# Performance work log

Hardware: AMD Instinct MI355X
Metric: run time of the kernel (lower is better)

Reference implementation:

```python
import jax, jax.numpy as jnp
import numpy as np

EPS = 1e-06

def setup_inputs() -> dict:
    key = jax.random.key(0)
    k1, k2, k3 = jax.random.split(key, 3)
    N, L, H, D = 4, 4096, 16, 64
    return {
        "queries": jax.random.normal(k1, (N, L, H, D), dtype=jnp.float32),
        "keys": jax.random.normal(k2, (N, L, H, D), dtype=jnp.float32),
        "values": jax.random.normal(k3, (N, L, H, D), dtype=jnp.float32),
    }

def reference(queries, keys, values):
    # [N, L, H, D] -> [N, H, L, D]
    q = jnp.transpose(queries, (0, 2, 1, 3))
    k = jnp.transpose(keys, (0, 2, 1, 3))
    v = jnp.transpose(values, (0, 2, 1, 3))
    # kernel feature map
    q = jax.nn.sigmoid(q)
    k = jax.nn.sigmoid(k)
    L = q.shape[2]
    S = k.shape[2]
    # incoming/outgoing flow normalizers
    normalizer_row = 1.0 / jnp.einsum('nhld,nhd->nhl', q + EPS, k.sum(axis=2) + EPS)
    normalizer_col = 1.0 / jnp.einsum('nhsd,nhd->nhs', k + EPS, q.sum(axis=2) + EPS)
    # refined normalizers (competition / allocation)
    row_refine = jnp.einsum('nhld,nhd->nhl', q + EPS,
                            (k * normalizer_col[..., None]).sum(axis=2) + EPS)
    col_refine = jnp.einsum('nhsd,nhd->nhs', k + EPS,
                            (q * normalizer_row[..., None]).sum(axis=2) + EPS)
    row_refine = jax.nn.sigmoid(row_refine * (float(L) / float(S)))
    col_refine = jax.nn.softmax(col_refine, axis=-1) * S
    # linear attention aggregation: kv is [N, H, D, D]
    kv = jnp.einsum('nhsd,nhse->nhde', k, v * col_refine[..., None])
    x = jnp.einsum('nhld,nhde->nhle', q, kv) * (normalizer_row * row_refine)[..., None]
    # back to [N, L, H, D]
    return jnp.transpose(x, (0, 2, 1, 3))
```

## Files before the change

### kernel.cpp

```cpp
#include <hip/hip_runtime.h>
#include <math.h>

#define EPS 1e-6f
constexpr int N_ = 4, L_ = 4096, H_ = 16, D_ = 64;
constexpr int NH = N_ * H_;
constexpr int HD = H_ * D_;
constexpr long NSTRIDE = (long)L_ * HD;
constexpr int SCHUNKS = 16;
constexpr int K1B = 1024;

typedef __attribute__((ext_vector_type(8))) short short8;
typedef __attribute__((ext_vector_type(4))) float f32x4;

__device__ float g_qsum[NH * D_];
__device__ float g_ksum[NH * D_];
__device__ float g_qnr[NH * D_];
__device__ float g_knc[NH * D_];
__device__ float g_ssum[NH];
__device__ float g_kv[NH * D_ * D_];
__device__ float g_kvpart[(long)SCHUNKS * NH * D_ * D_];
__device__ float g_part[2 * K1B * 1024];

__device__ __forceinline__ float sigm(float x) {
    return 1.0f / (1.0f + __expf(-x));
}
__device__ __forceinline__ float4 sigm4(float4 x) {
    float4 r;
    r.x = sigm(x.x); r.y = sigm(x.y); r.z = sigm(x.z); r.w = sigm(x.w);
    return r;
}
__device__ __forceinline__ float red16(float p) {
    p += __shfl_xor(p, 1);
    p += __shfl_xor(p, 2);
    p += __shfl_xor(p, 4);
    p += __shfl_xor(p, 8);
    return p;
}
__device__ __forceinline__ unsigned rne_hi(unsigned xb) {
    return (xb + 0x7fffu + ((xb >> 16) & 1u)) & 0xffff0000u;
}
__device__ __forceinline__ uint2 split2(float x) {
    unsigned h1 = rne_hi(__float_as_uint(x));
    float r = x - __uint_as_float(h1);
    unsigned h2 = rne_hi(__float_as_uint(r));
    return make_uint2(h1, h2);
}
union U8 { unsigned u[4]; short8 s; };

__global__ __launch_bounds__(256) void k1_sums(const float* __restrict__ q,
                                               const float* __restrict__ k) {
    const float* src = blockIdx.z ? k : q;
    int t = threadIdx.x;
    long g0 = (long)blockIdx.x * 16;
    const float* p = src + g0 * HD + t * 4;
    float ax = 0.f, ay = 0.f, az = 0.f, aw = 0.f;
#pragma unroll
    for (int r = 0; r < 16; ++r) {
        float4 x = *(const float4*)(p + (long)r * HD);
        float4 s = sigm4(x);
        ax += s.x; ay += s.y; az += s.z; aw += s.w;
    }
    float4 o = {ax, ay, az, aw};
    *(float4*)&g_part[((blockIdx.z * K1B + blockIdx.x) << 10) + t * 4] = o;
}

__global__ __launch_bounds__(256) void k2_norm(const float* __restrict__ q,
                                               const float* __restrict__ k) {
    bool col = blockIdx.z != 0;
    const float* src = col ? k : q;
    const float* sums = col ? g_qsum : g_ksum;
    int t = threadIdx.x;
    long g0 = (long)blockIdx.x * 16;
    int n = (int)(g0 >> 12);
    float4 bv = *(const float4*)(sums + n * 1024 + t * 4);
    bv.x += EPS; bv.y += EPS; bv.z += EPS; bv.w += EPS;
    const float* p = src + g0 * HD + t * 4;
    float ax = 0.f, ay = 0.f, az = 0.f, aw = 0.f;
#pragma unroll 4
    for (int r = 0; r < 16; ++r) {
        float4 x = *(const float4*)(p + (long)r * HD);
        float4 s = sigm4(x);
        float pd = (s.x + EPS) * bv.x + (s.y + EPS) * bv.y
                 + (s.z + EPS) * bv.z + (s.w + EPS) * bv.w;
        pd = red16(pd);
        float inv = 1.0f / pd;
        ax += s.x * inv; ay += s.y * inv; az += s.z * inv; aw += s.w * inv;
    }
    float4 o = {ax, ay, az, aw};
    *(float4*)&g_part[((blockIdx.z * K1B + blockIdx.x) << 10) + t * 4] = o;
}

__global__ __launch_bounds__(256) void kred(int which) {
    int bid = blockIdx.x, t = threadIdx.x;
    int z = bid & 1, n = (bid >> 1) & 3, cc = bid >> 3;
    int c = cc * 128 + (t & 31) * 4;
    int bg = t >> 5;
    float sx = 0.f, sy = 0.f, sz = 0.f, sw = 0.f;
#pragma unroll 4
    for (int i = 0; i < 32; ++i) {
        int b = n * 256 + bg * 32 + i;
        const float* pp = &g_part[((z * K1B + b) << 10) + c];
        float4 p = *(const float4*)pp;
        sx += p.x; sy += p.y; sz += p.z; sw += p.w;
    }
    __shared__ float4 esb[256];
    esb[t] = make_float4(sx, sy, sz, sw);
    __syncthreads();
    if (t < 32) {
        float4 s = esb[t];
#pragma unroll
        for (int g = 1; g < 8; ++g) {
            float4 b = esb[t + g * 32];
            s.x += b.x; s.y += b.y; s.z += b.z; s.w += b.w;
        }
        float* dst = which ? (z ? g_knc : g_qnr) : (z ? g_ksum : g_qsum);
        *(float4*)&dst[n * 1024 + cc * 128 + t * 4] = s;
    }
    if (which == 0 && bid == 0 && t < NH) g_ssum[t] = 0.f;
}

__global__ __launch_bounds__(256, 4) void k4_kv(const float* __restrict__ k,
                                                const float* __restrict__ v) {
    int nh = blockIdx.y, n = nh >> 4, h = nh & 15;
    int t = threadIdx.x, lane = t & 63, wv = t >> 6;
    __shared__ unsigned kA[16 * 66], kB[16 * 66], vA[16 * 66], vB[16 * 66];
    __shared__ float esb[256];
    int sp = t >> 4, c4 = t & 15;
    long nbase = (long)n * NSTRIDE + (long)h * D_;
    int s0blk = blockIdx.x * 256;
    float4 qn = *(const float4*)&g_qnr[nh * 64 + c4 * 4];
    qn.x += EPS; qn.y += EPS; qn.z += EPS; qn.w += EPS;

    f32x4 acc[4];
#pragma unroll
    for (int e = 0; e < 4; ++e) acc[e] = (f32x4){0.f, 0.f, 0.f, 0.f};
    int m = lane & 15, qd = lane >> 4;
    float esum = 0.f;

    float4 ke, ko, ve, vo;
    {
        long gb = nbase + (long)(s0blk + 2 * sp) * HD + c4 * 4;
        ke = *(const float4*)&k[gb]; ko = *(const float4*)&k[gb + HD];
        ve = *(const float4*)&v[gb]; vo = *(const float4*)&v[gb + HD];
    }
    for (int st = 0; st < 8; ++st) {
        float4 se = sigm4(ke), so = sigm4(ko);
        float pde = (se.x + EPS) * qn.x + (se.y + EPS) * qn.y
                  + (se.z + EPS) * qn.z + (se.w + EPS) * qn.w;
        float pdo = (so.x + EPS) * qn.x + (so.y + EPS) * qn.y
                  + (so.z + EPS) * qn.z + (so.w + EPS) * qn.w;
        pde = red16(pde); pdo = red16(pdo);
        float ee = __expf(pde), eo = __expf(pdo);
        if (c4 == 0) esum += ee + eo;
        se.x *= ee; se.y *= ee; se.z *= ee; se.w *= ee;
        so.x *= eo; so.y *= eo; so.z *= eo; so.w *= eo;
        uint2 a0 = split2(se.x), a1_ = split2(se.y), a2_ = split2(se.z), a3_ = split2(se.w);
        uint2 b0 = split2(so.x), b1_ = split2(so.y), b2_ = split2(so.z), b3_ = split2(so.w);
        unsigned kaw0 = (a0.x >> 16) | (b0.x & 0xffff0000u);
        unsigned kaw1 = (a1_.x >> 16) | (b1_.x & 0xffff0000u);
        unsigned kaw2 = (a2_.x >> 16) | (b2_.x & 0xffff0000u);
        unsigned kaw3 = (a3_.x >> 16) | (b3_.x & 0xffff0000u);
        unsigned kbw0 = (a0.y >> 16) | (b0.y & 0xffff0000u);
        unsigned kbw1 = (a1_.y >> 16) | (b1_.y & 0xffff0000u);
        unsigned kbw2 = (a2_.y >> 16) | (b2_.y & 0xffff0000u);
        unsigned kbw3 = (a3_.y >> 16) | (b3_.y & 0xffff0000u);
        uint2 c0 = split2(ve.x), c1 = split2(ve.y), c2 = split2(ve.z), c3 = split2(ve.w);
        uint2 d0 = split2(vo.x), d1 = split2(vo.y), d2 = split2(vo.z), d3 = split2(vo.w);
        unsigned vaw0 = (c0.x >> 16) | (d0.x & 0xffff0000u);
        unsigned vaw1 = (c1.x >> 16) | (d1.x & 0xffff0000u);
        unsigned vaw2 = (c2.x >> 16) | (d2.x & 0xffff0000u);
        unsigned vaw3 = (c3.x >> 16) | (d3.x & 0xffff0000u);
        unsigned vbw0 = (c0.y >> 16) | (d0.y & 0xffff0000u);
        unsigned vbw1 = (c1.y >> 16) | (d1.y & 0xffff0000u);
        unsigned vbw2 = (c2.y >> 16) | (d2.y & 0xffff0000u);
        unsigned vbw3 = (c3.y >> 16) | (d3.y & 0xffff0000u);
        __syncthreads();
        int wb = sp * 66 + c4 * 4;
        *(uint2*)&kA[wb] = make_uint2(kaw0, kaw1); *(uint2*)&kA[wb + 2] = make_uint2(kaw2, kaw3);
        *(uint2*)&kB[wb] = make_uint2(kbw0, kbw1); *(uint2*)&kB[wb + 2] = make_uint2(kbw2, kbw3);
        *(uint2*)&vA[wb] = make_uint2(vaw0, vaw1); *(uint2*)&vA[wb + 2] = make_uint2(vaw2, vaw3);
        *(uint2*)&vB[wb] = make_uint2(vbw0, vbw1); *(uint2*)&vB[wb + 2] = make_uint2(vbw2, vbw3);
        __syncthreads();
        if (st < 7) {
            long gb = nbase + (long)(s0blk + (st + 1) * 32 + 2 * sp) * HD + c4 * 4;
            ke = *(const float4*)&k[gb]; ko = *(const float4*)&k[gb + HD];
            ve = *(const float4*)&v[gb]; vo = *(const float4*)&v[gb + HD];
        }
        U8 fa1, fa2;
#pragma unroll
        for (int jp = 0; jp < 4; ++jp) {
            int idx = (qd * 4 + jp) * 66 + wv * 16 + m;
            fa1.u[jp] = kA[idx]; fa2.u[jp] = kB[idx];
        }
#pragma unroll
        for (int e = 0; e < 4; ++e) {
            U8 fb1, fb2;
#pragma unroll
            for (int jp = 0; jp < 4; ++jp) {
                int idx = (qd * 4 + jp) * 66 + e * 16 + m;
                fb1.u[jp] = vA[idx]; fb2.u[jp] = vB[idx];
            }
            acc[e] = __builtin_amdgcn_mfma_f32_16x16x32_bf16(fa1.s, fb2.s, acc[e], 0, 0, 0);
            acc[e] = __builtin_amdgcn_mfma_f32_16x16x32_bf16(fa2.s, fb1.s, acc[e], 0, 0, 0);
            acc[e] = __builtin_amdgcn_mfma_f32_16x16x32_bf16(fa1.s, fb1.s, acc[e], 0, 0, 0);
        }
    }
    float* dst = &g_kvpart[((long)blockIdx.x * NH + nh) * 4096];
#pragma unroll
    for (int e = 0; e < 4; ++e)
#pragma unroll
        for (int r = 0; r < 4; ++r)
            dst[(wv * 16 + qd * 4 + r) * 64 + e * 16 + m] = acc[e][r];
    esb[t] = esum;
    __syncthreads();
    for (int s = 128; s; s >>= 1) {
        if (t < s) esb[t] += esb[t + s];
        __syncthreads();
    }
    if (t == 0) atomicAdd(&g_ssum[nh], esb[0]);
}

__global__ __launch_bounds__(256) void k4b_reduce() {
    int nh = blockIdx.x;
    int i4 = blockIdx.y * 256 + threadIdx.x;
    float sx = 0.f, sy = 0.f, sz = 0.f, sw = 0.f;
#pragma unroll
    for (int c = 0; c < SCHUNKS; ++c) {
        float4 p = *(const float4*)&g_kvpart[((long)c * NH + nh) * 4096 + i4 * 4];
        sx += p.x; sy += p.y; sz += p.z; sw += p.w;
    }
    float scale = (float)L_ / g_ssum[nh];
    float4 o = {sx * scale, sy * scale, sz * scale, sw * scale};
    *(float4*)&g_kv[nh * 4096 + i4 * 4] = o;
}

__global__ __launch_bounds__(256, 4) void k5_out(const float* __restrict__ q,
                                                 float* __restrict__ out) {
    int nh = blockIdx.y, n = nh >> 4, h = nh & 15;
    int t = threadIdx.x, lane = t & 63, wv = t >> 6;
    __shared__ unsigned qA[32 * 66], qB[32 * 66], kvA[32 * 66], kvB[32 * 66];
    __shared__ float coef[64];
    int c4 = t & 15;
    long nbase = (long)n * NSTRIDE + (long)h * D_;
    int l0 = blockIdx.x * 64;
    float4 bk1 = *(const float4*)&g_ksum[nh * 64 + c4 * 4];
    float4 bk2 = *(const float4*)&g_knc[nh * 64 + c4 * 4];
    bk1.x += EPS; bk1.y += EPS; bk1.z += EPS; bk1.w += EPS;
    bk2.x += EPS; bk2.y += EPS; bk2.z += EPS; bk2.w += EPS;
#pragma unroll
    for (int j = 0; j < 2; ++j) {
        int slot = t + j * 256;
        int dp = slot >> 4, cc = slot & 15;
        const float* kvr = &g_kv[nh * 4096 + (2 * dp) * 64 + cc * 4];
        float4 xe = *(const float4*)kvr;
        float4 xo = *(const float4*)(kvr + 64);
        uint2 e0 = split2(xe.x), e1 = split2(xe.y), e2 = split2(xe.z), e3 = split2(xe.w);
        uint2 o0 = split2(xo.x), o1 = split2(xo.y), o2 = split2(xo.z), o3 = split2(xo.w);
        int wb = dp * 66 + cc * 4;
        *(uint2*)&kvA[wb] = make_uint2((e0.x >> 16) | (o0.x & 0xffff0000u),
                                       (e1.x >> 16) | (o1.x & 0xffff0000u));
        *(uint2*)&kvA[wb + 2] = make_uint2((e2.x >> 16) | (o2.x & 0xffff0000u),
                                           (e3.x >> 16) | (o3.x & 0xffff0000u));
        *(uint2*)&kvB[wb] = make_uint2((e0.y >> 16) | (o0.y & 0xffff0000u),
                                       (e1.y >> 16) | (o1.y & 0xffff0000u));
        *(uint2*)&kvB[wb + 2] = make_uint2((e2.y >> 16) | (o2.y & 0xffff0000u),
                                           (e3.y >> 16) | (o3.y & 0xffff0000u));
    }
#pragma unroll
    for (int j = 0; j < 4; ++j) {
        int slot = t + j * 256;
        int r = slot >> 4;
        float4 x = *(const float4*)&q[nbase + (long)(l0 + r) * HD + c4 * 4];
        float4 s = sigm4(x);
        float p1 = (s.x + EPS) * bk1.x + (s.y + EPS) * bk1.y
                 + (s.z + EPS) * bk1.z + (s.w + EPS) * bk1.w;
        float p2 = (s.x + EPS) * bk2.x + (s.y + EPS) * bk2.y
                 + (s.z + EPS) * bk2.z + (s.w + EPS) * bk2.w;
        p1 = red16(p1); p2 = red16(p2);
        if (c4 == 0) coef[r] = sigm(p2) / p1;
        uint2 t0 = split2(s.x), t1 = split2(s.y), t2 = split2(s.z), t3 = split2(s.w);
        qA[(c4 * 2) * 66 + r]     = (t0.x >> 16) | (t1.x & 0xffff0000u);
        qB[(c4 * 2) * 66 + r]     = (t0.y >> 16) | (t1.y & 0xffff0000u);
        qA[(c4 * 2 + 1) * 66 + r] = (t2.x >> 16) | (t3.x & 0xffff0000u);
        qB[(c4 * 2 + 1) * 66 + r] = (t2.y >> 16) | (t3.y & 0xffff0000u);
    }
    __syncthreads();
    int m = lane & 15, qd = lane >> 4;
    f32x4 acc[4];
#pragma unroll
    for (int e = 0; e < 4; ++e) acc[e] = (f32x4){0.f, 0.f, 0.f, 0.f};
#pragma unroll
    for (int kk = 0; kk < 2; ++kk) {
        U8 fa1, fa2;
#pragma unroll
        for (int jp = 0; jp < 4; ++jp) {
            int idx = (kk * 16 + qd * 4 + jp) * 66 + wv * 16 + m;
            fa1.u[jp] = qA[idx]; fa2.u[jp] = qB[idx];
        }
#pragma unroll
        for (int e = 0; e < 4; ++e) {
            U8 fb1, fb2;
#pragma unroll
            for (int jp = 0; jp < 4; ++jp) {
                int idx = (kk * 16 + qd * 4 + jp) * 66 + e * 16 + m;
                fb1.u[jp] = kvA[idx]; fb2.u[jp] = kvB[idx];
            }
            acc[e] = __builtin_amdgcn_mfma_f32_16x16x32_bf16(fa1.s, fb2.s, acc[e], 0, 0, 0);
            acc[e] = __builtin_amdgcn_mfma_f32_16x16x32_bf16(fa2.s, fb1.s, acc[e], 0, 0, 0);
            acc[e] = __builtin_amdgcn_mfma_f32_16x16x32_bf16(fa1.s, fb1.s, acc[e], 0, 0, 0);
        }
    }
#pragma unroll
    for (int e = 0; e < 4; ++e)
#pragma unroll
        for (int r = 0; r < 4; ++r) {
            int ll = wv * 16 + qd * 4 + r;
            out[nbase + (long)(l0 + ll) * HD + e * 16 + m] = acc[e][r] * coef[ll];
        }
}

extern "C" void kernel_launch(void* const* d_in, const int* in_sizes, int n_in,
                              void* d_out, int out_size, void* d_ws, size_t ws_size,
                              hipStream_t stream) {
    const float* q = (const float*)d_in[0];
    const float* k = (const float*)d_in[1];
    const float* v = (const float*)d_in[2];
    float* out = (float*)d_out;

    k1_sums<<<dim3(K1B, 1, 2), 256, 0, stream>>>(q, k);
    kred<<<64, 256, 0, stream>>>(0);
    k2_norm<<<dim3(K1B, 1, 2), 256, 0, stream>>>(q, k);
    kred<<<64, 256, 0, stream>>>(1);
    k4_kv<<<dim3(SCHUNKS, NH), 256, 0, stream>>>(k, v);
    k4b_reduce<<<dim3(NH, 4), 256, 0, stream>>>();
    k5_out<<<dim3(L_ / 64, NH), 256, 0, stream>>>(q, out);
}
```

Measured before the change: 292.5 us.

## Fuse column-normalizer pass into KV kernel and drop redundant q/k sweeps

Restructures the stage schedule. The q-sum and row-normalizer sums are computed in one pass over q, and the k-sum is computed alone. The column-normalizer sum over k, previously a separate full read of k, is now computed inside the KV kernel, which already reads k. Per-chunk partials replace the atomic for the softmax denominator, and the output kernel hoists its global loads ahead of the conversion math. The aim is to cut two full-tensor reads of q/k from the normalizer stages, at the cost of extra ALU and register pressure in the KV kernel.

After: 281.0 us. 4.0% less time.

```diff
diff --git a/kernel.cpp b/kernel.cpp
--- a/kernel.cpp
+++ b/kernel.cpp
@@ -7,7 +7,7 @@
 constexpr int HD = H_ * D_;
 constexpr long NSTRIDE = (long)L_ * HD;
 constexpr int SCHUNKS = 16;
-constexpr int K1B = 1024;
+constexpr int KSB = 2048;
 
 typedef __attribute__((ext_vector_type(8))) short short8;
 typedef __attribute__((ext_vector_type(4))) float f32x4;
@@ -16,10 +16,13 @@
 __device__ float g_ksum[NH * D_];
 __device__ float g_qnr[NH * D_];
 __device__ float g_knc[NH * D_];
-__device__ float g_ssum[NH];
 __device__ float g_kv[NH * D_ * D_];
 __device__ float g_kvpart[(long)SCHUNKS * NH * D_ * D_];
-__device__ float g_part[2 * K1B * 1024];
+__device__ float g_kncpart[SCHUNKS * NH * D_];
+__device__ float g_ssumpart[SCHUNKS * NH];
+__device__ float g_partK[(long)KSB * 1024];
+__device__ float g_partQs[(long)KSB * 1024];
+__device__ float g_partQn[(long)KSB * 1024];
 
 __device__ __forceinline__ float sigm(float x) {
     return 1.0f / (1.0f + __expf(-x));
@@ -47,60 +50,63 @@
 }
 union U8 { unsigned u[4]; short8 s; };
 
-__global__ __launch_bounds__(256) void k1_sums(const float* __restrict__ q,
-                                               const float* __restrict__ k) {
-    const float* src = blockIdx.z ? k : q;
+__global__ __launch_bounds__(256, 8) void kA_ksum(const float* __restrict__ k) {
     int t = threadIdx.x;
-    long g0 = (long)blockIdx.x * 16;
-    const float* p = src + g0 * HD + t * 4;
+    long g0 = (long)blockIdx.x * 8;
+    const float* p = k + g0 * HD + t * 4;
+    float4 x[8];
+#pragma unroll
+    for (int r = 0; r < 8; ++r) x[r] = *(const float4*)(p + (long)r * HD);
     float ax = 0.f, ay = 0.f, az = 0.f, aw = 0.f;
 #pragma unroll
-    for (int r = 0; r < 16; ++r) {
-        float4 x = *(const float4*)(p + (long)r * HD);
-        float4 s = sigm4(x);
+    for (int r = 0; r < 8; ++r) {
+        float4 s = sigm4(x[r]);
         ax += s.x; ay += s.y; az += s.z; aw += s.w;
     }
     float4 o = {ax, ay, az, aw};
-    *(float4*)&g_part[((blockIdx.z * K1B + blockIdx.x) << 10) + t * 4] = o;
-}
-
-__global__ __launch_bounds__(256) void k2_norm(const float* __restrict__ q,
-                                               const float* __restrict__ k) {
-    bool col = blockIdx.z != 0;
-    const float* src = col ? k : q;
-    const float* sums = col ? g_qsum : g_ksum;
+    *(float4*)&g_partK[((long)blockIdx.x << 10) + t * 4] = o;
+}
+
+__global__ __launch_bounds__(256, 8) void kB_q(const float* __restrict__ q) {
     int t = threadIdx.x;
-    long g0 = (long)blockIdx.x * 16;
+    long g0 = (long)blockIdx.x * 8;
     int n = (int)(g0 >> 12);
-    float4 bv = *(const float4*)(sums + n * 1024 + t * 4);
+    float4 bv = *(const float4*)(g_ksum + n * 1024 + t * 4);
     bv.x += EPS; bv.y += EPS; bv.z += EPS; bv.w += EPS;
-    const float* p = src + g0 * HD + t * 4;
-    float ax = 0.f, ay = 0.f, az = 0.f, aw = 0.f;
-#pragma unroll 4
-    for (int r = 0; r < 16; ++r) {
-        float4 x = *(const float4*)(p + (long)r * HD);
-        float4 s = sigm4(x);
+    const float* p = q + g0 * HD + t * 4;
+    float4 x[8];
+#pragma unroll
+    for (int r = 0; r < 8; ++r) x[r] = *(const float4*)(p + (long)r * HD);
+    float sx = 0.f, sy = 0.f, sz = 0.f, sw = 0.f;
+    float nx = 0.f, ny = 0.f, nz = 0.f, nw = 0.f;
+#pragma unroll
+    for (int r = 0; r < 8; ++r) {
+        float4 s = sigm4(x[r]);
+        sx += s.x; sy += s.y; sz += s.z; sw += s.w;
         float pd = (s.x + EPS) * bv.x + (s.y + EPS) * bv.y
                  + (s.z + EPS) * bv.z + (s.w + EPS) * bv.w;
         pd = red16(pd);
         float inv = 1.0f / pd;
-        ax += s.x * inv; ay += s.y * inv; az += s.z * inv; aw += s.w * inv;
-    }
-    float4 o = {ax, ay, az, aw};
-    *(float4*)&g_part[((blockIdx.z * K1B + blockIdx.x) << 10) + t * 4] = o;
-}
-
-__global__ __launch_bounds__(256) void kred(int which) {
-    int bid = blockIdx.x, t = threadIdx.x;
-    int z = bid & 1, n = (bid >> 1) & 3, cc = bid >> 3;
+        nx += s.x * inv; ny += s.y * inv; nz += s.z * inv; nw += s.w * inv;
+    }
+    float4 os = {sx, sy, sz, sw};
+    float4 on = {nx, ny, nz, nw};
+    *(float4*)&g_partQs[((long)blockIdx.x << 10) + t * 4] = os;
+    *(float4*)&g_partQn[((long)blockIdx.x << 10) + t * 4] = on;
+}
+
+__global__ __launch_bounds__(256) void kred(int mode) {
+    int t = threadIdx.x, z = blockIdx.y;
+    const float* src = (mode == 0) ? g_partK : (z ? g_partQn : g_partQs);
+    float* dst = (mode == 0) ? g_ksum : (z ? g_qnr : g_qsum);
+    int n = blockIdx.x & 3, cc = blockIdx.x >> 2;
     int c = cc * 128 + (t & 31) * 4;
     int bg = t >> 5;
     float sx = 0.f, sy = 0.f, sz = 0.f, sw = 0.f;
 #pragma unroll 4
-    for (int i = 0; i < 32; ++i) {
-        int b = n * 256 + bg * 32 + i;
-        const float* pp = &g_part[((z * K1B + b) << 10) + c];
-        float4 p = *(const float4*)pp;
+    for (int i = 0; i < 64; ++i) {
+        long b = n * 512 + bg * 64 + i;
+        float4 p = *(const float4*)&src[(b << 10) + c];
         sx += p.x; sy += p.y; sz += p.z; sw += p.w;
     }
     __shared__ float4 esb[256];
@@ -110,13 +116,11 @@
         float4 s = esb[t];
 #pragma unroll
         for (int g = 1; g < 8; ++g) {
-            float4 b = esb[t + g * 32];
-            s.x += b.x; s.y += b.y; s.z += b.z; s.w += b.w;
-        }
-        float* dst = which ? (z ? g_knc : g_qnr) : (z ? g_ksum : g_qsum);
+            float4 b2 = esb[t + g * 32];
+            s.x += b2.x; s.y += b2.y; s.z += b2.z; s.w += b2.w;
+        }
         *(float4*)&dst[n * 1024 + cc * 128 + t * 4] = s;
     }
-    if (which == 0 && bid == 0 && t < NH) g_ssum[t] = 0.f;
 }
 
 __global__ __launch_bounds__(256, 4) void k4_kv(const float* __restrict__ k,
@@ -124,18 +128,22 @@
     int nh = blockIdx.y, n = nh >> 4, h = nh & 15;
     int t = threadIdx.x, lane = t & 63, wv = t >> 6;
     __shared__ unsigned kA[16 * 66], kB[16 * 66], vA[16 * 66], vB[16 * 66];
+    __shared__ float kncred[16 * 64];
     __shared__ float esb[256];
     int sp = t >> 4, c4 = t & 15;
     long nbase = (long)n * NSTRIDE + (long)h * D_;
     int s0blk = blockIdx.x * 256;
     float4 qn = *(const float4*)&g_qnr[nh * 64 + c4 * 4];
     qn.x += EPS; qn.y += EPS; qn.z += EPS; qn.w += EPS;
+    float4 qs = *(const float4*)&g_qsum[nh * 64 + c4 * 4];
+    qs.x += EPS; qs.y += EPS; qs.z += EPS; qs.w += EPS;
 
     f32x4 acc[4];
 #pragma unroll
     for (int e = 0; e < 4; ++e) acc[e] = (f32x4){0.f, 0.f, 0.f, 0.f};
     int m = lane & 15, qd = lane >> 4;
     float esum = 0.f;
+    float knx = 0.f, kny = 0.f, knz = 0.f, knw = 0.f;
 
     float4 ke, ko, ve, vo;
     {
@@ -149,9 +157,19 @@
                   + (se.z + EPS) * qn.z + (se.w + EPS) * qn.w;
         float pdo = (so.x + EPS) * qn.x + (so.y + EPS) * qn.y
                   + (so.z + EPS) * qn.z + (so.w + EPS) * qn.w;
+        float pne = (se.x + EPS) * qs.x + (se.y + EPS) * qs.y
+                  + (se.z + EPS) * qs.z + (se.w + EPS) * qs.w;
+        float pno = (so.x + EPS) * qs.x + (so.y + EPS) * qs.y
+                  + (so.z + EPS) * qs.z + (so.w + EPS) * qs.w;
         pde = red16(pde); pdo = red16(pdo);
+        pne = red16(pne); pno = red16(pno);
         float ee = __expf(pde), eo = __expf(pdo);
         if (c4 == 0) esum += ee + eo;
+        float nce = 1.0f / pne, nco = 1.0f / pno;
+        knx += se.x * nce + so.x * nco;
+        kny += se.y * nce + so.y * nco;
+        knz += se.z * nce + so.z * nco;
+        knw += se.w * nce + so.w * nco;
         se.x *= ee; se.y *= ee; se.z *= ee; se.w *= ee;
         so.x *= eo; so.y *= eo; so.z *= eo; so.w *= eo;
         uint2 a0 = split2(se.x), a1_ = split2(se.y), a2_ = split2(se.z), a3_ = split2(se.w);
@@ -211,27 +229,43 @@
 #pragma unroll
         for (int r = 0; r < 4; ++r)
             dst[(wv * 16 + qd * 4 + r) * 64 + e * 16 + m] = acc[e][r];
+    *(float4*)&kncred[sp * 64 + c4 * 4] = make_float4(knx, kny, knz, knw);
     esb[t] = esum;
     __syncthreads();
-    for (int s = 128; s; s >>= 1) {
-        if (t < s) esb[t] += esb[t + s];
+    if (t < 64) {
+        float s = 0.f;
+#pragma unroll
+        for (int i = 0; i < 16; ++i) s += kncred[i * 64 + t];
+        g_kncpart[(blockIdx.x * NH + nh) * 64 + t] = s;
+    }
+    for (int s2 = 128; s2; s2 >>= 1) {
+        if (t < s2) esb[t] += esb[t + s2];
         __syncthreads();
     }
-    if (t == 0) atomicAdd(&g_ssum[nh], esb[0]);
+    if (t == 0) g_ssumpart[blockIdx.x * NH + nh] = esb[0];
 }
 
 __global__ __launch_bounds__(256) void k4b_reduce() {
-    int nh = blockIdx.x;
-    int i4 = blockIdx.y * 256 + threadIdx.x;
+    int nh = blockIdx.x, t = threadIdx.x;
+    float ssum = 0.f;
+#pragma unroll
+    for (int c = 0; c < SCHUNKS; ++c) ssum += g_ssumpart[c * NH + nh];
+    float scale = (float)L_ / ssum;
+    int i4 = blockIdx.y * 256 + t;
     float sx = 0.f, sy = 0.f, sz = 0.f, sw = 0.f;
 #pragma unroll
     for (int c = 0; c < SCHUNKS; ++c) {
         float4 p = *(const float4*)&g_kvpart[((long)c * NH + nh) * 4096 + i4 * 4];
         sx += p.x; sy += p.y; sz += p.z; sw += p.w;
     }
-    float scale = (float)L_ / g_ssum[nh];
     float4 o = {sx * scale, sy * scale, sz * scale, sw * scale};
     *(float4*)&g_kv[nh * 4096 + i4 * 4] = o;
+    if (blockIdx.y == 0 && t < 64) {
+        float s = 0.f;
+#pragma unroll
+        for (int c = 0; c < SCHUNKS; ++c) s += g_kncpart[(c * NH + nh) * 64 + t];
+        g_knc[nh * 64 + t] = s;
+    }
 }
 
 __global__ __launch_bounds__(256, 4) void k5_out(const float* __restrict__ q,
@@ -247,15 +281,27 @@
     float4 bk2 = *(const float4*)&g_knc[nh * 64 + c4 * 4];
     bk1.x += EPS; bk1.y += EPS; bk1.z += EPS; bk1.w += EPS;
     bk2.x += EPS; bk2.y += EPS; bk2.z += EPS; bk2.w += EPS;
+    float4 xe[2], xo[2];
 #pragma unroll
     for (int j = 0; j < 2; ++j) {
         int slot = t + j * 256;
         int dp = slot >> 4, cc = slot & 15;
         const float* kvr = &g_kv[nh * 4096 + (2 * dp) * 64 + cc * 4];
-        float4 xe = *(const float4*)kvr;
-        float4 xo = *(const float4*)(kvr + 64);
-        uint2 e0 = split2(xe.x), e1 = split2(xe.y), e2 = split2(xe.z), e3 = split2(xe.w);
-        uint2 o0 = split2(xo.x), o1 = split2(xo.y), o2 = split2(xo.z), o3 = split2(xo.w);
+        xe[j] = *(const float4*)kvr;
+        xo[j] = *(const float4*)(kvr + 64);
+    }
+    float4 xq[4];
+#pragma unroll
+    for (int j = 0; j < 4; ++j) {
+        int r = (t >> 4) + j * 16;
+        xq[j] = *(const float4*)&q[nbase + (long)(l0 + r) * HD + c4 * 4];
+    }
+#pragma unroll
+    for (int j = 0; j < 2; ++j) {
+        int slot = t + j * 256;
+        int dp = slot >> 4, cc = slot & 15;
+        uint2 e0 = split2(xe[j].x), e1 = split2(xe[j].y), e2 = split2(xe[j].z), e3 = split2(xe[j].w);
+        uint2 o0 = split2(xo[j].x), o1 = split2(xo[j].y), o2 = split2(xo[j].z), o3 = split2(xo[j].w);
         int wb = dp * 66 + cc * 4;
         *(uint2*)&kvA[wb] = make_uint2((e0.x >> 16) | (o0.x & 0xffff0000u),
                                        (e1.x >> 16) | (o1.x & 0xffff0000u));
@@ -268,10 +314,8 @@
     }
 #pragma unroll
     for (int j = 0; j < 4; ++j) {
-        int slot = t + j * 256;
-        int r = slot >> 4;
-        float4 x = *(const float4*)&q[nbase + (long)(l0 + r) * HD + c4 * 4];
-        float4 s = sigm4(x);
+        int r = (t >> 4) + j * 16;
+        float4 s = sigm4(xq[j]);
         float p1 = (s.x + EPS) * bk1.x + (s.y + EPS) * bk1.y
                  + (s.z + EPS) * bk1.z + (s.w + EPS) * bk1.w;
         float p2 = (s.x + EPS) * bk2.x + (s.y + EPS) * bk2.y
@@ -327,10 +371,10 @@
     const float* v = (const float*)d_in[2];
     float* out = (float*)d_out;
 
-    k1_sums<<<dim3(K1B, 1, 2), 256, 0, stream>>>(q, k);
-    kred<<<64, 256, 0, stream>>>(0);
-    k2_norm<<<dim3(K1B, 1, 2), 256, 0, stream>>>(q, k);
-    kred<<<64, 256, 0, stream>>>(1);
+    kA_ksum<<<KSB, 256, 0, stream>>>(k);
+    kred<<<dim3(32, 1), 256, 0, stream>>>(0);
+    kB_q<<<KSB, 256, 0, stream>>>(q);
+    kred<<<dim3(32, 2), 256, 0, stream>>>(1);
     k4_kv<<<dim3(SCHUNKS, NH), 256, 0, stream>>>(k, v);
     k4b_reduce<<<dim3(NH, 4), 256, 0, stream>>>();
     k5_out<<<dim3(L_ / 64, NH), 256, 0, stream>>>(q, out);
```
